# Performance work log

Hardware: AMD Instinct MI355X
Metric: run time of the kernel (lower is better)

Reference implementation:

```python
import jax, jax.numpy as jnp
import numpy as np

B, L, HP, H, W = 4, 32, 32, 64, 64
D, DFFN, MAXL = 32, 64, 128

def setup_inputs() -> dict:
    key = jax.random.key(0)
    ks = jax.random.split(key, 20)
    rn = lambda k, s, sc=0.1: jax.random.normal(k, s, jnp.float32) * sc
    return {
        'x': jax.random.normal(ks[0], (B, 2 * L * HP, H, W), jnp.float32),
        'in_proj_w': rn(ks[1], (D, 12)), 'in_proj_b': rn(ks[2], (D,)),
        'layer_emb': rn(ks[3], (MAXL, D)),
        'time_decay': rn(ks[4], (D,)), 'time_first': rn(ks[5], (D,)),
        'ln_tm_g': jnp.ones((D,)), 'ln_tm_b': jnp.zeros((D,)),
        'tm_r': rn(ks[6], (D, D)), 'tm_k': rn(ks[7], (D, D)),
        'tm_v': rn(ks[8], (D, D)), 'tm_out': rn(ks[9], (D, D)),
        'ln_cm_g': jnp.ones((D,)), 'ln_cm_b': jnp.zeros((D,)),
        'cm_k': rn(ks[10], (DFFN, D)), 'cm_v': rn(ks[11], (D, DFFN)), 'cm_r': rn(ks[12], (D, D)),
        'gate_w': rn(ks[13], (1, D)), 'gate_b': rn(ks[14], (1,)),
        'row_w': rn(ks[15], (H, D)), 'row_b': rn(ks[16], (H,)),
        'col_w': rn(ks[17], (W, D)), 'col_b': rn(ks[18], (W,)),
    }

def _ln(x, g, b, eps=1e-5):
    mu = x.mean(-1, keepdims=True)
    var = ((x - mu) ** 2).mean(-1, keepdims=True)
    return (x - mu) * jax.lax.rsqrt(var + eps) * g + b

def _stats(a, b):
    # a, b: [B, L, HP, H, W] -> [B, L, HP, 12]
    af = a.reshape(*a.shape[:-2], -1)
    bf = b.reshape(*b.shape[:-2], -1)
    hs = lambda f: jnp.stack([f.mean(-1), f.std(-1, ddof=1), f.min(-1), f.max(-1)], -1)
    d = af - bf
    dm = d.mean(-1, keepdims=True)
    ds = d.std(-1, ddof=1, keepdims=True)
    dl2 = jnp.linalg.norm(d, axis=-1, keepdims=True)
    na = jnp.maximum(jnp.linalg.norm(af, axis=-1), 1e-8)
    nb = jnp.maximum(jnp.linalg.norm(bf, axis=-1), 1e-8)
    cos = ((af * bf).sum(-1) / (na * nb))[..., None]
    return jnp.concatenate([hs(af), hs(bf), dm, ds, dl2, cos], -1)

def reference(x, in_proj_w, in_proj_b, layer_emb, time_decay, time_first,
              ln_tm_g, ln_tm_b, tm_r, tm_k, tm_v, tm_out,
              ln_cm_g, ln_cm_b, cm_k, cm_v, cm_r,
              gate_w, gate_b, row_w, row_b, col_w, col_b):
    n = L * HP
    a = x[:, :n].reshape(B, L, HP, H, W)
    b = x[:, n:].reshape(B, L, HP, H, W)
    stats = _stats(a, b)                                   # [B,L,HP,12]
    feat_in = jnp.einsum('blhs,ds->blhd', stats, in_proj_w) + in_proj_b \
        + layer_emb[:L][None, :, None, :]
    feat_in = jnp.transpose(feat_in, (1, 0, 2, 3))         # [L,B,HP,D]
    wdec = jnp.exp(time_decay)

    def step(state, f):
        aa, bb, pp = state
        xn = _ln(f, ln_tm_g, ln_tm_b)
        r = jax.nn.sigmoid(xn @ tm_r.T)
        k = xn @ tm_k.T
        v = xn @ tm_v.T
        ww = time_first + k
        p = jnp.maximum(pp, ww)
        e1 = jnp.exp(pp - p)
        e2 = jnp.exp(ww - p)
        wkv = (e1 * aa + e2 * v) / jnp.maximum(e1 * bb + e2, 1e-8)
        ww2 = pp - wdec
        p2 = jnp.maximum(ww2, k)
        e1b = jnp.exp(ww2 - p2)
        e2b = jnp.exp(k - p2)
        y = f + r * (wkv @ tm_out.T)
        xn2 = _ln(y, ln_cm_g, ln_cm_b)
        kk = jnp.square(jax.nn.relu(xn2 @ cm_k.T))
        y = y + jax.nn.sigmoid(xn2 @ cm_r.T) * (kk @ cm_v.T)
        return (e1b * aa + e2b * v, e1b * bb + e2b, p2), y

    z = jnp.zeros((B, HP, D), x.dtype)
    init = (z, z, jnp.full((B, HP, D), -1e30, x.dtype))
    _, feats = jax.lax.scan(step, init, feat_in)           # [L,B,HP,D]

    gate = feats @ gate_w.T + gate_b                       # [L,B,HP,1]
    row = feats @ row_w.T + row_b                          # [L,B,HP,H]
    col = feats @ col_w.T + col_b                          # [L,B,HP,W]
    mask = jax.nn.sigmoid(gate[..., None] + row[..., None] + col[..., None, :])
    aT = jnp.transpose(a, (1, 0, 2, 3, 4))
    bT = jnp.transpose(b, (1, 0, 2, 3, 4))
    merged = mask * aT + (1.0 - mask) * bT                 # [L,B,HP,H,W]
    mixed = jnp.transpose(merged, (1, 0, 2, 3, 4)).reshape(B, n, H, W)
    return mixed, jax.nn.sigmoid(gate).mean(), mask.mean()
```

## Files before the change

### kernel.cpp

```cpp
#include <hip/hip_runtime.h>
#include <math.h>


__device__ __forceinline__ float sigf(float v) { return 1.0f / (1.0f + __expf(-v)); }

__global__ __launch_bounds__(256, 4) void k_stats(
    const float* __restrict__ x, const float* __restrict__ in_proj_w,
    const float* __restrict__ in_proj_b, const float* __restrict__ layer_emb,
    const float* __restrict__ ln_tm_g, const float* __restrict__ ln_tm_b,
    const float* __restrict__ tm_r, const float* __restrict__ tm_k,
    const float* __restrict__ tm_v,
    float* __restrict__ f_out, float* __restrict__ r_out,
    float* __restrict__ kv_out)
{
    __shared__ float red[4][9];
    __shared__ __align__(16) float xn_s[32];
    const int bid = blockIdx.x;
    const int hp = bid & 31, l = (bid >> 5) & 31, bb = bid >> 10;
    const float4* pa = (const float4*)(x + (size_t)(bb * 2048 + l * 32 + hp) * 4096);
    const float4* pb = (const float4*)(x + (size_t)(bb * 2048 + 1024 + l * 32 + hp) * 4096);
    const int t = threadIdx.x;
    const int gidx = ((l * 4 + bb) * 32 + hp) * 32;

    float sa = 0.f, saa = 0.f, sb = 0.f, sbb = 0.f, sab = 0.f;
    float mna = 3.4e38f, mxa = -3.4e38f, mnb = 3.4e38f, mxb = -3.4e38f;
#pragma unroll
    for (int it = 0; it < 4; ++it) {
        float4 a4 = pa[t + it * 256];
        float4 b4 = pb[t + it * 256];
        sa  += a4.x + a4.y + a4.z + a4.w;
        sb  += b4.x + b4.y + b4.z + b4.w;
        saa += a4.x * a4.x + a4.y * a4.y + a4.z * a4.z + a4.w * a4.w;
        sbb += b4.x * b4.x + b4.y * b4.y + b4.z * b4.z + b4.w * b4.w;
        sab += a4.x * b4.x + a4.y * b4.y + a4.z * b4.z + a4.w * b4.w;
        mna = fminf(mna, fminf(fminf(a4.x, a4.y), fminf(a4.z, a4.w)));
        mxa = fmaxf(mxa, fmaxf(fmaxf(a4.x, a4.y), fmaxf(a4.z, a4.w)));
        mnb = fminf(mnb, fminf(fminf(b4.x, b4.y), fminf(b4.z, b4.w)));
        mxb = fmaxf(mxb, fmaxf(fmaxf(b4.x, b4.y), fmaxf(b4.z, b4.w)));
    }
#pragma unroll
    for (int m = 1; m < 64; m <<= 1) {
        sa  += __shfl_xor(sa, m);
        saa += __shfl_xor(saa, m);
        sb  += __shfl_xor(sb, m);
        sbb += __shfl_xor(sbb, m);
        sab += __shfl_xor(sab, m);
        mna = fminf(mna, __shfl_xor(mna, m));
        mxa = fmaxf(mxa, __shfl_xor(mxa, m));
        mnb = fminf(mnb, __shfl_xor(mnb, m));
        mxb = fmaxf(mxb, __shfl_xor(mxb, m));
    }
    const int lane = t & 63, wv = t >> 6;
    if (lane == 0) {
        red[wv][0] = sa;  red[wv][1] = saa; red[wv][2] = sb;  red[wv][3] = sbb;
        red[wv][4] = sab; red[wv][5] = mna; red[wv][6] = mxa; red[wv][7] = mnb;
        red[wv][8] = mxb;
    }
    __syncthreads();
    if (t < 64) {
        if (t < 32) {
            const float SA  = red[0][0] + red[1][0] + red[2][0] + red[3][0];
            const float SAA = red[0][1] + red[1][1] + red[2][1] + red[3][1];
            const float SB  = red[0][2] + red[1][2] + red[2][2] + red[3][2];
            const float SBB = red[0][3] + red[1][3] + red[2][3] + red[3][3];
            const float SAB = red[0][4] + red[1][4] + red[2][4] + red[3][4];
            const float MNA = fminf(fminf(red[0][5], red[1][5]), fminf(red[2][5], red[3][5]));
            const float MXA = fmaxf(fmaxf(red[0][6], red[1][6]), fmaxf(red[2][6], red[3][6]));
            const float MNB = fminf(fminf(red[0][7], red[1][7]), fminf(red[2][7], red[3][7]));
            const float MXB = fmaxf(fmaxf(red[0][8], red[1][8]), fmaxf(red[2][8], red[3][8]));
            const float inv_n = 1.f / 4096.f, inv_nm1 = 1.f / 4095.f;
            float st[12];
            st[0] = SA * inv_n;
            st[1] = sqrtf(fmaxf(SAA - SA * SA * inv_n, 0.f) * inv_nm1);
            st[2] = MNA; st[3] = MXA;
            st[4] = SB * inv_n;
            st[5] = sqrtf(fmaxf(SBB - SB * SB * inv_n, 0.f) * inv_nm1);
            st[6] = MNB; st[7] = MXB;
            const float SD = SA - SB, SDD = SAA - 2.f * SAB + SBB;
            st[8]  = SD * inv_n;
            st[9]  = sqrtf(fmaxf(SDD - SD * SD * inv_n, 0.f) * inv_nm1);
            st[10] = sqrtf(fmaxf(SDD, 0.f));
            const float na = fmaxf(sqrtf(SAA), 1e-8f), nb2 = fmaxf(sqrtf(SBB), 1e-8f);
            st[11] = SAB / (na * nb2);
            float fv = in_proj_b[t] + layer_emb[l * 32 + t];
#pragma unroll
            for (int s2 = 0; s2 < 12; ++s2) fv += st[s2] * in_proj_w[t * 12 + s2];
            f_out[gidx + t] = fv;
            float s = fv, q = fv * fv;
#pragma unroll
            for (int m = 1; m < 32; m <<= 1) { s += __shfl_xor(s, m, 32); q += __shfl_xor(q, m, 32); }
            const float mu = s * (1.f / 32.f);
            const float var = fmaxf(q * (1.f / 32.f) - mu * mu, 0.f);
            xn_s[t] = (fv - mu) * rsqrtf(var + 1e-5f) * ln_tm_g[t] + ln_tm_b[t];
        }
        const int d = t & 31;
        const float4* x4 = (const float4*)xn_s;
        const float4* w1 = (const float4*)((t < 32 ? tm_r : tm_k) + d * 32);
        float a0 = 0.f, a1 = 0.f, a2 = 0.f, a3 = 0.f;
#pragma unroll
        for (int jq = 0; jq < 2; ++jq) {
            float4 w, xv;
            w = w1[jq];     xv = x4[jq];     a0 += w.x*xv.x + w.y*xv.y + w.z*xv.z + w.w*xv.w;
            w = w1[jq + 2]; xv = x4[jq + 2]; a1 += w.x*xv.x + w.y*xv.y + w.z*xv.z + w.w*xv.w;
            w = w1[jq + 4]; xv = x4[jq + 4]; a2 += w.x*xv.x + w.y*xv.y + w.z*xv.z + w.w*xv.w;
            w = w1[jq + 6]; xv = x4[jq + 6]; a3 += w.x*xv.x + w.y*xv.y + w.z*xv.z + w.w*xv.w;
        }
        const float dot1 = (a0 + a1) + (a2 + a3);
        if (t < 32) {
            r_out[gidx + d] = sigf(dot1);
            const float4* w2 = (const float4*)(tm_v + d * 32);
            float b0 = 0.f, b1 = 0.f, b2 = 0.f, b3 = 0.f;
#pragma unroll
            for (int jq = 0; jq < 2; ++jq) {
                float4 w, xv;
                w = w2[jq];     xv = x4[jq];     b0 += w.x*xv.x + w.y*xv.y + w.z*xv.z + w.w*xv.w;
                w = w2[jq + 2]; xv = x4[jq + 2]; b1 += w.x*xv.x + w.y*xv.y + w.z*xv.z + w.w*xv.w;
                w = w2[jq + 4]; xv = x4[jq + 4]; b2 += w.x*xv.x + w.y*xv.y + w.z*xv.z + w.w*xv.w;
                w = w2[jq + 6]; xv = x4[jq + 6]; b3 += w.x*xv.x + w.y*xv.y + w.z*xv.z + w.w*xv.w;
            }
            kv_out[2 * (gidx + d) + 1] = (b0 + b1) + (b2 + b3);
        } else {
            kv_out[2 * (gidx + d)] = dot1;
        }
    }
}

__global__ __launch_bounds__(64) void k_wkv(
    const float* __restrict__ kv_in,
    const float* __restrict__ time_decay, const float* __restrict__ time_first,
    float* __restrict__ wkv_out)
{
    const int ch = blockIdx.x * 64 + threadIdx.x;
    const int d = ch & 31;
    const float tf = time_first[d];
    const float wd = __expf(time_decay[d]);
    const float2* kv2 = (const float2*)kv_in;
    float2 kv[32];
#pragma unroll
    for (int l = 0; l < 32; ++l) kv[l] = kv2[l * 4096 + ch];
    float aa = 0.f, bbs = 0.f, pp = -1e30f;
#pragma unroll
    for (int l = 0; l < 32; ++l) {
        const float kc = kv[l].x, vc = kv[l].y;
        const float ww = tf + kc;
        const float p = fmaxf(pp, ww);
        const float e1 = __expf(pp - p), e2 = __expf(ww - p);
        wkv_out[l * 4096 + ch] = (e1 * aa + e2 * vc) / fmaxf(e1 * bbs + e2, 1e-8f);
        const float ww2 = pp - wd;
        const float p2 = fmaxf(ww2, kc);
        const float e1b = __expf(ww2 - p2), e2b = __expf(kc - p2);
        aa = e1b * aa + e2b * vc;
        bbs = e1b * bbs + e2b;
        pp = p2;
    }
}

__global__ __launch_bounds__(256, 4) void k_merge(
    const float* __restrict__ x,
    const float* __restrict__ f_in, const float* __restrict__ r_in,
    const float* __restrict__ wkv_in,
    const float* __restrict__ tm_out,
    const float* __restrict__ ln_cm_g, const float* __restrict__ ln_cm_b,
    const float* __restrict__ cm_k, const float* __restrict__ cm_v,
    const float* __restrict__ cm_r,
    const float* __restrict__ gate_w, const float* __restrict__ gate_b,
    const float* __restrict__ row_w, const float* __restrict__ row_b,
    const float* __restrict__ col_w, const float* __restrict__ col_b,
    float* __restrict__ out, float* __restrict__ gpart, float* __restrict__ mpart)
{
    __shared__ __align__(16) float wkv_s[32];
    __shared__ __align__(16) float xn2_s[32];
    __shared__ __align__(16) float kk_s[64];
    __shared__ __align__(16) float fs[32];
    __shared__ float row_s[64], col_s[64];
    __shared__ float gate_sh;
    __shared__ float red2[4];
    const int bid = blockIdx.x;
    const int hp = bid & 31, l = (bid >> 5) & 31, bb = bid >> 10;
    const int t = threadIdx.x;
    const int gidx = ((l * 4 + bb) * 32 + hp) * 32;

    const float4* pa = (const float4*)(x + (size_t)(bb * 2048 + l * 32 + hp) * 4096);
    const float4* pb = (const float4*)(x + (size_t)(bb * 2048 + 1024 + l * 32 + hp) * 4096);
    float4* po = (float4*)(out + (size_t)(bb * 1024 + l * 32 + hp) * 4096);

    if (t < 64) {
        float yv = 0.f, y2 = 0.f;
        if (t < 32) {
            wkv_s[t] = wkv_in[gidx + t];
            const float fv = f_in[gidx + t];
            const float rv = r_in[gidx + t];
            const float4* w4 = (const float4*)(tm_out + t * 32);
            const float4* x4 = (const float4*)wkv_s;
            float a0 = 0.f, a1 = 0.f, a2 = 0.f, a3 = 0.f;
#pragma unroll
            for (int jq = 0; jq < 2; ++jq) {
                float4 w, xv;
                w = w4[jq];     xv = x4[jq];     a0 += w.x*xv.x + w.y*xv.y + w.z*xv.z + w.w*xv.w;
                w = w4[jq + 2]; xv = x4[jq + 2]; a1 += w.x*xv.x + w.y*xv.y + w.z*xv.z + w.w*xv.w;
                w = w4[jq + 4]; xv = x4[jq + 4]; a2 += w.x*xv.x + w.y*xv.y + w.z*xv.z + w.w*xv.w;
                w = w4[jq + 6]; xv = x4[jq + 6]; a3 += w.x*xv.x + w.y*xv.y + w.z*xv.z + w.w*xv.w;
            }
            yv = fv + rv * ((a0 + a1) + (a2 + a3));
            float s = yv, q = yv * yv;
#pragma unroll
            for (int m = 1; m < 32; m <<= 1) { s += __shfl_xor(s, m, 32); q += __shfl_xor(q, m, 32); }
            const float mu = s * (1.f / 32.f);
            const float var = fmaxf(q * (1.f / 32.f) - mu * mu, 0.f);
            xn2_s[t] = (yv - mu) * rsqrtf(var + 1e-5f) * ln_cm_g[t] + ln_cm_b[t];
        }
        {
            const float4* w4 = (const float4*)(cm_k + t * 32);
            const float4* x4 = (const float4*)xn2_s;
            float a0 = 0.f, a1 = 0.f, a2 = 0.f, a3 = 0.f;
#pragma unroll
            for (int jq = 0; jq < 2; ++jq) {
                float4 w, xv;
                w = w4[jq];     xv = x4[jq];     a0 += w.x*xv.x + w.y*xv.y + w.z*xv.z + w.w*xv.w;
                w = w4[jq + 2]; xv = x4[jq + 2]; a1 += w.x*xv.x + w.y*xv.y + w.z*xv.z + w.w*xv.w;
                w = w4[jq + 4]; xv = x4[jq + 4]; a2 += w.x*xv.x + w.y*xv.y + w.z*xv.z + w.w*xv.w;
                w = w4[jq + 6]; xv = x4[jq + 6]; a3 += w.x*xv.x + w.y*xv.y + w.z*xv.z + w.w*xv.w;
            }
            float kk = fmaxf((a0 + a1) + (a2 + a3), 0.f);
            kk_s[t] = kk * kk;
        }
        if (t < 32) {
            float cr;
            {
                const float4* w4 = (const float4*)(cm_r + t * 32);
                const float4* x4 = (const float4*)xn2_s;
                float a0 = 0.f, a1 = 0.f, a2 = 0.f, a3 = 0.f;
#pragma unroll
                for (int jq = 0; jq < 2; ++jq) {
                    float4 w, xv;
                    w = w4[jq];     xv = x4[jq];     a0 += w.x*xv.x + w.y*xv.y + w.z*xv.z + w.w*xv.w;
                    w = w4[jq + 2]; xv = x4[jq + 2]; a1 += w.x*xv.x + w.y*xv.y + w.z*xv.z + w.w*xv.w;
                    w = w4[jq + 4]; xv = x4[jq + 4]; a2 += w.x*xv.x + w.y*xv.y + w.z*xv.z + w.w*xv.w;
                    w = w4[jq + 6]; xv = x4[jq + 6]; a3 += w.x*xv.x + w.y*xv.y + w.z*xv.z + w.w*xv.w;
                }
                cr = sigf((a0 + a1) + (a2 + a3));
            }
            {
                const float4* w4 = (const float4*)(cm_v + t * 64);
                const float4* x4 = (const float4*)kk_s;
                float a0 = 0.f, a1 = 0.f, a2 = 0.f, a3 = 0.f;
#pragma unroll
                for (int jq = 0; jq < 4; ++jq) {
                    float4 w, xv;
                    w = w4[jq];      xv = x4[jq];      a0 += w.x*xv.x + w.y*xv.y + w.z*xv.z + w.w*xv.w;
                    w = w4[jq + 4];  xv = x4[jq + 4];  a1 += w.x*xv.x + w.y*xv.y + w.z*xv.z + w.w*xv.w;
                    w = w4[jq + 8];  xv = x4[jq + 8];  a2 += w.x*xv.x + w.y*xv.y + w.z*xv.z + w.w*xv.w;
                    w = w4[jq + 12]; xv = x4[jq + 12]; a3 += w.x*xv.x + w.y*xv.y + w.z*xv.z + w.w*xv.w;
                }
                y2 = yv + cr * ((a0 + a1) + (a2 + a3));
            }
            fs[t] = y2;
            float g = y2 * gate_w[t];
#pragma unroll
            for (int m = 1; m < 32; m <<= 1) g += __shfl_xor(g, m, 32);
            if (t == 0) gate_sh = g + gate_b[0];
        }
        {
            float a0 = row_b[t], a1 = 0.f, a2 = 0.f, a3 = 0.f;
            float c0 = col_b[t], c1 = 0.f, c2 = 0.f, c3 = 0.f;
#pragma unroll
            for (int d2 = 0; d2 < 8; ++d2) {
                const float f0 = fs[d2], f1 = fs[d2 + 8], f2 = fs[d2 + 16], f3 = fs[d2 + 24];
                a0 += f0 * row_w[t * 32 + d2];
                a1 += f1 * row_w[t * 32 + d2 + 8];
                a2 += f2 * row_w[t * 32 + d2 + 16];
                a3 += f3 * row_w[t * 32 + d2 + 24];
                c0 += f0 * col_w[t * 32 + d2];
                c1 += f1 * col_w[t * 32 + d2 + 8];
                c2 += f2 * col_w[t * 32 + d2 + 16];
                c3 += f3 * col_w[t * 32 + d2 + 24];
            }
            row_s[t] = (a0 + a1) + (a2 + a3);
            col_s[t] = (c0 + c1) + (c2 + c3);
        }
    }
    __syncthreads();

    const float gate = gate_sh;
    float msum = 0.f;
#pragma unroll
    for (int it = 0; it < 4; ++it) {
        const int i = t + it * 256;
        const float4 a4 = pa[i];
        const float4 b4 = pb[i];
        const int h = i >> 4, w0 = (i & 15) * 4;
        const float gr = gate + row_s[h];
        const float m0 = sigf(gr + col_s[w0 + 0]);
        const float m1 = sigf(gr + col_s[w0 + 1]);
        const float m2 = sigf(gr + col_s[w0 + 2]);
        const float m3 = sigf(gr + col_s[w0 + 3]);
        float4 o;
        o.x = b4.x + m0 * (a4.x - b4.x);
        o.y = b4.y + m1 * (a4.y - b4.y);
        o.z = b4.z + m2 * (a4.z - b4.z);
        o.w = b4.w + m3 * (a4.w - b4.w);
        po[i] = o;
        msum += m0 + m1 + m2 + m3;
    }
#pragma unroll
    for (int m = 1; m < 64; m <<= 1) msum += __shfl_xor(msum, m);
    if ((t & 63) == 0) red2[t >> 6] = msum;
    __syncthreads();
    if (t == 0) {
        mpart[bid] = red2[0] + red2[1] + red2[2] + red2[3];
        gpart[bid] = sigf(gate);
    }
}

__global__ __launch_bounds__(256) void k_final(
    const float* __restrict__ gpart, const float* __restrict__ mpart,
    float* __restrict__ out)
{
    __shared__ float rg[4], rm[4];
    const int t = threadIdx.x;
    float gs = 0.f, ms = 0.f;
    for (int i = t; i < 4096; i += 256) { gs += gpart[i]; ms += mpart[i]; }
#pragma unroll
    for (int m = 1; m < 64; m <<= 1) { gs += __shfl_xor(gs, m); ms += __shfl_xor(ms, m); }
    if ((t & 63) == 0) { rg[t >> 6] = gs; rm[t >> 6] = ms; }
    __syncthreads();
    if (t == 0) {
        out[16777216] = (rg[0] + rg[1] + rg[2] + rg[3]) * (1.f / 4096.f);
        out[16777217] = (rm[0] + rm[1] + rm[2] + rm[3]) * (1.f / 16777216.f);
    }
}

extern "C" void kernel_launch(void* const* d_in, const int* in_sizes, int n_in,
                              void* d_out, int out_size, void* d_ws, size_t ws_size,
                              hipStream_t stream) {
    const float* x          = (const float*)d_in[0];
    const float* in_proj_w  = (const float*)d_in[1];
    const float* in_proj_b  = (const float*)d_in[2];
    const float* layer_emb  = (const float*)d_in[3];
    const float* time_decay = (const float*)d_in[4];
    const float* time_first = (const float*)d_in[5];
    const float* ln_tm_g    = (const float*)d_in[6];
    const float* ln_tm_b    = (const float*)d_in[7];
    const float* tm_r       = (const float*)d_in[8];
    const float* tm_k       = (const float*)d_in[9];
    const float* tm_v       = (const float*)d_in[10];
    const float* tm_out     = (const float*)d_in[11];
    const float* ln_cm_g    = (const float*)d_in[12];
    const float* ln_cm_b    = (const float*)d_in[13];
    const float* cm_k       = (const float*)d_in[14];
    const float* cm_v       = (const float*)d_in[15];
    const float* cm_r       = (const float*)d_in[16];
    const float* gate_w     = (const float*)d_in[17];
    const float* gate_b     = (const float*)d_in[18];
    const float* row_w      = (const float*)d_in[19];
    const float* row_b      = (const float*)d_in[20];
    const float* col_w      = (const float*)d_in[21];
    const float* col_b      = (const float*)d_in[22];
    float* out = (float*)d_out;

    float* wsf    = (float*)d_ws;
    float* f_ws   = wsf;
    float* r_ws   = wsf + 131072;
    float* kv_ws  = wsf + 262144;
    float* wkv_ws = wsf + 524288;
    float* gpart  = wsf + 655360;
    float* mpart  = wsf + 659456;

    k_stats<<<dim3(4096), dim3(256), 0, stream>>>(
        x, in_proj_w, in_proj_b, layer_emb, ln_tm_g, ln_tm_b,
        tm_r, tm_k, tm_v, f_ws, r_ws, kv_ws);
    k_wkv<<<dim3(64), dim3(64), 0, stream>>>(
        kv_ws, time_decay, time_first, wkv_ws);
    k_merge<<<dim3(4096), dim3(256), 0, stream>>>(
        x, f_ws, r_ws, wkv_ws, tm_out, ln_cm_g, ln_cm_b, cm_k, cm_v, cm_r,
        gate_w, gate_b, row_w, row_b, col_w, col_b, out, gpart, mpart);
    k_final<<<dim3(1), dim3(256), 0, stream>>>(gpart, mpart, out);
}
```

Before: 300.9 us.

## Fuse WKV scan into merge kernel by recomputing prefix per block

Removes the separate tiny sequential WKV kernel (64 blocks of 64 threads) and its intermediate buffer. Each merge block now recomputes the recurrence over layers 0..l for its own 32 channels, reading all 32 layers of kv from the workspace. This drops one launch and the serialized low-occupancy scan stage, at the cost of redundant work: each block loads 32 float2 values per channel and runs up to 32 scan steps before starting the merge.

```diff
diff --git a/kernel.cpp b/kernel.cpp
--- a/kernel.cpp
+++ b/kernel.cpp
@@ -125,40 +125,11 @@
     }
 }
 
-__global__ __launch_bounds__(64) void k_wkv(
+__global__ __launch_bounds__(256, 4) void k_fused(
+    const float* __restrict__ x,
+    const float* __restrict__ f_in, const float* __restrict__ r_in,
     const float* __restrict__ kv_in,
     const float* __restrict__ time_decay, const float* __restrict__ time_first,
-    float* __restrict__ wkv_out)
-{
-    const int ch = blockIdx.x * 64 + threadIdx.x;
-    const int d = ch & 31;
-    const float tf = time_first[d];
-    const float wd = __expf(time_decay[d]);
-    const float2* kv2 = (const float2*)kv_in;
-    float2 kv[32];
-#pragma unroll
-    for (int l = 0; l < 32; ++l) kv[l] = kv2[l * 4096 + ch];
-    float aa = 0.f, bbs = 0.f, pp = -1e30f;
-#pragma unroll
-    for (int l = 0; l < 32; ++l) {
-        const float kc = kv[l].x, vc = kv[l].y;
-        const float ww = tf + kc;
-        const float p = fmaxf(pp, ww);
-        const float e1 = __expf(pp - p), e2 = __expf(ww - p);
-        wkv_out[l * 4096 + ch] = (e1 * aa + e2 * vc) / fmaxf(e1 * bbs + e2, 1e-8f);
-        const float ww2 = pp - wd;
-        const float p2 = fmaxf(ww2, kc);
-        const float e1b = __expf(ww2 - p2), e2b = __expf(kc - p2);
-        aa = e1b * aa + e2b * vc;
-        bbs = e1b * bbs + e2b;
-        pp = p2;
-    }
-}
-
-__global__ __launch_bounds__(256, 4) void k_merge(
-    const float* __restrict__ x,
-    const float* __restrict__ f_in, const float* __restrict__ r_in,
-    const float* __restrict__ wkv_in,
     const float* __restrict__ tm_out,
     const float* __restrict__ ln_cm_g, const float* __restrict__ ln_cm_b,
     const float* __restrict__ cm_k, const float* __restrict__ cm_v,
@@ -178,7 +149,8 @@
     const int bid = blockIdx.x;
     const int hp = bid & 31, l = (bid >> 5) & 31, bb = bid >> 10;
     const int t = threadIdx.x;
-    const int gidx = ((l * 4 + bb) * 32 + hp) * 32;
+    const int chb = bb * 1024 + hp * 32;
+    const int gidx = l * 4096 + chb;
 
     const float4* pa = (const float4*)(x + (size_t)(bb * 2048 + l * 32 + hp) * 4096);
     const float4* pb = (const float4*)(x + (size_t)(bb * 2048 + 1024 + l * 32 + hp) * 4096);
@@ -187,7 +159,30 @@
     if (t < 64) {
         float yv = 0.f, y2 = 0.f;
         if (t < 32) {
-            wkv_s[t] = wkv_in[gidx + t];
+            const float2* kv2p = (const float2*)kv_in;
+            float2 kv[32];
+#pragma unroll
+            for (int l2 = 0; l2 < 32; ++l2) kv[l2] = kv2p[l2 * 4096 + chb + t];
+            const float tf = time_first[t];
+            const float wd = __expf(time_decay[t]);
+            float aa = 0.f, bbs = 0.f, pp = -1e30f, wkv = 0.f;
+#pragma unroll
+            for (int l2 = 0; l2 < 32; ++l2) {
+                if (l2 < l) {
+                    const float ww2 = pp - wd;
+                    const float p2 = fmaxf(ww2, kv[l2].x);
+                    const float e1b = __expf(ww2 - p2), e2b = __expf(kv[l2].x - p2);
+                    aa = e1b * aa + e2b * kv[l2].y;
+                    bbs = e1b * bbs + e2b;
+                    pp = p2;
+                } else if (l2 == l) {
+                    const float ww = tf + kv[l2].x;
+                    const float p = fmaxf(pp, ww);
+                    const float e1 = __expf(pp - p), e2 = __expf(ww - p);
+                    wkv = (e1 * aa + e2 * kv[l2].y) / fmaxf(e1 * bbs + e2, 1e-8f);
+                }
+            }
+            wkv_s[t] = wkv;
             const float fv = f_in[gidx + t];
             const float rv = r_in[gidx + t];
             const float4* w4 = (const float4*)(tm_out + t * 32);
@@ -362,17 +357,15 @@
     float* f_ws   = wsf;
     float* r_ws   = wsf + 131072;
     float* kv_ws  = wsf + 262144;
-    float* wkv_ws = wsf + 524288;
-    float* gpart  = wsf + 655360;
-    float* mpart  = wsf + 659456;
+    float* gpart  = wsf + 524288;
+    float* mpart  = wsf + 528384;
 
     k_stats<<<dim3(4096), dim3(256), 0, stream>>>(
         x, in_proj_w, in_proj_b, layer_emb, ln_tm_g, ln_tm_b,
         tm_r, tm_k, tm_v, f_ws, r_ws, kv_ws);
-    k_wkv<<<dim3(64), dim3(64), 0, stream>>>(
-        kv_ws, time_decay, time_first, wkv_ws);
-    k_merge<<<dim3(4096), dim3(256), 0, stream>>>(
-        x, f_ws, r_ws, wkv_ws, tm_out, ln_cm_g, ln_cm_b, cm_k, cm_v, cm_r,
+    k_fused<<<dim3(4096), dim3(256), 0, stream>>>(
+        x, f_ws, r_ws, kv_ws, time_decay, time_first, tm_out,
+        ln_cm_g, ln_cm_b, cm_k, cm_v, cm_r,
         gate_w, gate_b, row_w, row_b, col_w, col_b, out, gpart, mpart);
     k_final<<<dim3(1), dim3(256), 0, stream>>>(gpart, mpart, out);
 }
```

New measurement: 299.1 us. No clear change (-0.6%).
